# Performance work log

Measured on AMD Instinct MI355X. Metric: run time of the kernel, lower is better.

Reference implementation:

```python
import jax, jax.numpy as jnp
import numpy as np

N_BASIS = 128   # n_atom_basis F
N_INT   = 3     # n_interactions
N_RBF   = 20
CUTOFF  = 5.0
MAX_Z   = 100
EPS     = 1e-8
N_ATOMS = 25000
N_EDGES = 200000


def setup_inputs() -> dict:
    key = jax.random.key(0)
    ks = jax.random.split(key, 16)
    F = N_BASIS
    s = 0.02
    z     = jax.random.randint(ks[0], (N_ATOMS,), 1, MAX_Z)
    pos   = jax.random.uniform(ks[1], (N_ATOMS, 3), dtype=jnp.float32) * 2.0  # small box -> inside cutoff
    idx_i = jax.random.randint(ks[2], (N_EDGES,), 0, N_ATOMS)
    idx_j = jax.random.randint(ks[3], (N_EDGES,), 0, N_ATOMS)
    emb   = jax.random.normal(ks[4], (MAX_Z, F), dtype=jnp.float32) * s
    fW    = jax.random.normal(ks[5], (N_RBF, 3 * F * N_INT), dtype=jnp.float32) * s
    fb    = jnp.zeros((3 * F * N_INT,), jnp.float32)
    iW1   = jax.random.normal(ks[6], (N_INT, F, F), dtype=jnp.float32) * s
    ib1   = jnp.zeros((N_INT, F), jnp.float32)
    iW2   = jax.random.normal(ks[7], (N_INT, F, 3 * F), dtype=jnp.float32) * s
    ib2   = jnp.zeros((N_INT, 3 * F), jnp.float32)
    mWmix = jax.random.normal(ks[8], (N_INT, F, 2 * F), dtype=jnp.float32) * s
    mW1   = jax.random.normal(ks[9], (N_INT, 2 * F, F), dtype=jnp.float32) * s
    mb1   = jnp.zeros((N_INT, F), jnp.float32)
    mW2   = jax.random.normal(ks[10], (N_INT, F, 3 * F), dtype=jnp.float32) * s
    mb2   = jnp.zeros((N_INT, 3 * F), jnp.float32)
    return dict(z=z, pos=pos, idx_i=idx_i, idx_j=idx_j, emb=emb, fW=fW, fb=fb,
                iW1=iW1, ib1=ib1, iW2=iW2, ib2=ib2,
                mWmix=mWmix, mW1=mW1, mb1=mb1, mW2=mW2, mb2=mb2)


def reference(z, pos, idx_i, idx_j, emb, fW, fb, iW1, ib1, iW2, ib2,
              mWmix, mW1, mb1, mW2, mb2):
    F = N_BASIS
    n_atoms = z.shape[0]
    # geometry
    r_ij = pos[idx_j] - pos[idx_i]                                  # [E,3]
    r_ij = jnp.where(jnp.abs(r_ij) < 1e-6, 1e-6, r_ij)
    d_ij = jnp.linalg.norm(r_ij, axis=1, keepdims=True)             # [E,1]
    dir_ij = r_ij / d_ij                                            # [E,3]
    # Gaussian radial basis
    offsets = jnp.linspace(0.0, CUTOFF, N_RBF)
    width = offsets[1] - offsets[0]
    coeff = -0.5 / (width * width)
    phi = jnp.exp(coeff * (d_ij[..., None] - offsets) ** 2)         # [E,1,n_rbf]
    # cosine cutoff
    fcut = 0.5 * (jnp.cos(jnp.pi * d_ij / CUTOFF) + 1.0) * (d_ij < CUTOFF)  # [E,1]
    filters = (phi @ fW + fb) * fcut[..., None]                     # [E,1,3F*I]
    filter_list = jnp.split(filters, N_INT, axis=-1)                # each [E,1,3F]
    # initial atom features
    q = emb[z][:, None, :]                                          # [N,1,F]
    mu = jnp.zeros((n_atoms, 3, F), q.dtype)                        # [N,3,F]
    for t in range(N_INT):
        # --- interaction (gather - filter-multiply - scatter-add) ---
        x = jax.nn.silu(q @ iW1[t] + ib1[t]) @ iW2[t] + ib2[t]      # [N,1,3F]
        xj = x[idx_j]                                               # [E,1,3F]
        muj = mu[idx_j]                                             # [E,3,F]
        x = filter_list[t] * xj                                     # [E,1,3F]
        dq, dmuR, dmumu = jnp.split(x, 3, axis=-1)                  # [E,1,F] each
        dq = jax.ops.segment_sum(dq, idx_i, num_segments=n_atoms)   # [N,1,F]
        dmu = dmuR * dir_ij[..., None] + dmumu * muj                # [E,3,F]
        dmu = jax.ops.segment_sum(dmu, idx_i, num_segments=n_atoms) # [N,3,F]
        q = q + dq
        mu = mu + dmu
        # --- mixing (intra-atomic) ---
        mu_mix = mu @ mWmix[t]                                      # [N,3,2F]
        mu_V, mu_W = jnp.split(mu_mix, 2, axis=-1)                  # [N,3,F]
        mu_Vn = jnp.sqrt(jnp.sum(mu_V ** 2, axis=-2, keepdims=True) + EPS)  # [N,1,F]
        ctx = jnp.concatenate([q, mu_Vn], axis=-1)                  # [N,1,2F]
        x = jax.nn.silu(ctx @ mW1[t] + mb1[t]) @ mW2[t] + mb2[t]    # [N,1,3F]
        dq_intra, dmu_intra, dqmu_intra = jnp.split(x, 3, axis=-1)
        dmu_intra = dmu_intra * mu_W                                # [N,3,F]
        dqmu_intra = dqmu_intra * jnp.sum(mu_V * mu_W, axis=1, keepdims=True)
        q = q + dq_intra + dqmu_intra
        mu = mu + dmu_intra
    return q.squeeze(1), mu
```

## Files before the change

kernel.cpp:

```cpp
#include <hip/hip_runtime.h>
#include <hip/hip_bf16.h>

#define F 128
#define F3 384
#define NRBF 20
#define NITER 3
#define KP 24

typedef __hip_bfloat16 bf16;
typedef __bf16 bfrag __attribute__((ext_vector_type(8)));
typedef float f32x4 __attribute__((ext_vector_type(4)));

__device__ __forceinline__ float b2f(bf16 v) { return __bfloat162float(v); }
__device__ __forceinline__ bf16 f2b(float v) { return __float2bfloat16(v); }
__device__ __forceinline__ bfrag ldb(const bf16* p) { return *(const bfrag*)p; }
__device__ __forceinline__ bfrag ldsb(const __bf16* p) { return *(const bfrag*)p; }
__device__ __forceinline__ bfrag cvtf(const float* p) {
    bfrag r;
#pragma unroll
    for (int j = 0; j < 8; ++j) r[j] = (__bf16)p[j];
    return r;
}

__global__ void detect_kernel(const unsigned short* __restrict__ raw, int n_u16,
                              int* __restrict__ flag) {
    int i = blockIdx.x * blockDim.x + threadIdx.x;
    int bad = 0;
    for (int k = i; k < n_u16; k += blockDim.x * gridDim.x) {
        unsigned e = (raw[k] >> 7) & 0xFFu;
        if (e >= 140u) bad = 1;
    }
    if (bad) atomicOr(flag, 1);
}

struct CvtArgs {
    const void* src[13];
    float* dst[13];
    int end[14];
};
__global__ void cvt_all_kernel(CvtArgs a, const int* __restrict__ flag, int total) {
    int idx = blockIdx.x * blockDim.x + threadIdx.x;
    if (idx >= total) return;
    int s = 0;
    while (idx >= a.end[s + 1]) ++s;
    int local = idx - a.end[s];
    float v = (*flag) ? ((const float*)a.src[s])[local]
                      : b2f(((const bf16*)a.src[s])[local]);
    a.dst[s][local] = v;
}

struct TpArgs {
    const float* src[5];
    bf16* dst[5];
    int K[5];
    int Nn[5];
    int end[6];
};
__global__ void tpose_all_kernel(TpArgs a, int total) {
    int idx = blockIdx.x * blockDim.x + threadIdx.x;
    if (idx >= total) return;
    int s = 0;
    while (idx >= a.end[s + 1]) ++s;
    int local = idx - a.end[s];
    int K = a.K[s], Nn = a.Nn[s], slice = K * Nn;
    int t = local / slice, j = local - t * slice;
    int n = j / K, k = j - n * K;
    a.dst[s][local] = f2b(a.src[s][t * slice + k * Nn + n]);
}

__global__ void fwt_kernel(const float* __restrict__ fW, const float* __restrict__ fb,
                           float* __restrict__ dst, int total) {
    int idx = blockIdx.x * blockDim.x + threadIdx.x;
    if (idx >= total) return;
    int k = idx % KP, rest = idx / KP;
    int n = rest % F3, t = rest / F3;
    float v = (k < NRBF) ? fW[k * (F3 * NITER) + t * F3 + n]
                         : (k == NRBF ? fb[t * F3 + n] : 0.0f);
    dst[idx] = v;
}

__global__ void geom_kernel(const float* __restrict__ pos, const int* __restrict__ ii,
                            const int* __restrict__ jj, const int* __restrict__ rank,
                            bf16* __restrict__ phifc2, float* __restrict__ dir2, int E) {
    int e = blockIdx.x * blockDim.x + threadIdx.x;
    if (e >= E) return;
    int i = ii[e], j = jj[e], l = rank[e];
    float r[3];
#pragma unroll
    for (int d = 0; d < 3; ++d) {
        float v = pos[j * 3 + d] - pos[i * 3 + d];
        if (fabsf(v) < 1e-6f) v = 1e-6f;
        r[d] = v;
    }
    float dd = sqrtf(r[0] * r[0] + r[1] * r[1] + r[2] * r[2]);
    float inv = 1.0f / dd;
#pragma unroll
    for (int d = 0; d < 3; ++d) dir2[(size_t)l * 4 + d] = r[d] * inv;
    dir2[(size_t)l * 4 + 3] = __int_as_float(j);
    const float CUT = 5.0f;
    const float PI = 3.14159265358979323846f;
    float fc = (dd < CUT) ? 0.5f * (cosf(PI * dd / CUT) + 1.0f) : 0.0f;
    const float width = CUT / (NRBF - 1);
    const float coeff = -0.5f / (width * width);
    bf16* pr = phifc2 + (size_t)l * KP;
#pragma unroll
    for (int k = 0; k < NRBF; ++k) {
        float diff = dd - (float)k * width;
        pr[k] = f2b(expf(coeff * diff * diff) * fc);
    }
    pr[NRBF] = f2b(fc);
    pr[NRBF + 1] = f2b(0.0f);
    pr[NRBF + 2] = f2b(0.0f);
    pr[NRBF + 3] = f2b(0.0f);
}

__global__ void embed_kernel(const int* __restrict__ z, const float* __restrict__ emb,
                             float* __restrict__ q, int N) {
    int idx = blockIdx.x * blockDim.x + threadIdx.x;
    if (idx >= N * F) return;
    int n = idx >> 7, f = idx & 127;
    q[idx] = emb[z[n] * F + f];
}

__global__ void count_kernel(const int* __restrict__ ii, int* __restrict__ counts, int E) {
    int e = blockIdx.x * blockDim.x + threadIdx.x;
    if (e < E) atomicAdd(&counts[ii[e]], 1);
}

__global__ void scan_kernel(const int* __restrict__ counts, int* __restrict__ offs, int N) {
    __shared__ int cum[1024];
    int t = threadIdx.x;
    int chunk = (N + 1023) >> 10;
    int b = t * chunk;
    int e = b + chunk; if (e > N) e = N;
    int s = 0;
    for (int a = b; a < e; ++a) s += counts[a];
    cum[t] = s;
    __syncthreads();
    for (int o = 1; o < 1024; o <<= 1) {
        int u = (t >= o) ? cum[t - o] : 0;
        __syncthreads();
        cum[t] += u;
        __syncthreads();
    }
    int run = cum[t] - s;
    for (int a = b; a < e; ++a) { offs[a] = run; run += counts[a]; }
    if (t == 1023) offs[N] = cum[1023];
}

__global__ void fill_kernel(const int* __restrict__ ii, const int* __restrict__ offs,
                            int* __restrict__ cursor, int* __restrict__ rank, int E) {
    int e = blockIdx.x * blockDim.x + threadIdx.x;
    if (e >= E) return;
    int i = ii[e];
    int p = atomicAdd(&cursor[i], 1);
    rank[e] = offs[i] + p;
}

__global__ __launch_bounds__(256) void atom_x_mfma(
    const float* __restrict__ q, const bf16* __restrict__ W1T, const float* __restrict__ b1,
    const bf16* __restrict__ W2T, const float* __restrict__ b2, bf16* __restrict__ x, int N) {
    __shared__ __bf16 H[32][136];
    int tid = threadIdx.x;
    int w = tid >> 6, l = tid & 63;
    int lm = l & 15, q4 = l >> 4;
    int i0 = blockIdx.x * 32;
    f32x4 acc[2][2] = {};
    int r0 = min(i0 + lm, N - 1);
    int r1 = min(i0 + 16 + lm, N - 1);
    for (int kt = 0; kt < 4; ++kt) {
        int ko = kt * 32 + q4 * 8;
        bfrag a0 = cvtf(q + (size_t)r0 * F + ko);
        bfrag a1 = cvtf(q + (size_t)r1 * F + ko);
        bfrag b0 = ldb(W1T + (size_t)(w * 32 + lm) * F + ko);
        bfrag b1f = ldb(W1T + (size_t)(w * 32 + 16 + lm) * F + ko);
        acc[0][0] = __builtin_amdgcn_mfma_f32_16x16x32_bf16(a0, b0, acc[0][0], 0, 0, 0);
        acc[1][0] = __builtin_amdgcn_mfma_f32_16x16x32_bf16(a1, b0, acc[1][0], 0, 0, 0);
        acc[0][1] = __builtin_amdgcn_mfma_f32_16x16x32_bf16(a0, b1f, acc[0][1], 0, 0, 0);
        acc[1][1] = __builtin_amdgcn_mfma_f32_16x16x32_bf16(a1, b1f, acc[1][1], 0, 0, 0);
    }
#pragma unroll
    for (int nt = 0; nt < 2; ++nt) {
        int col = w * 32 + nt * 16 + lm;
        float bb = b1[col];
#pragma unroll
        for (int mt = 0; mt < 2; ++mt)
#pragma unroll
            for (int r = 0; r < 4; ++r) {
                float v = acc[mt][nt][r] + bb;
                H[mt * 16 + q4 * 4 + r][col] = (__bf16)(v / (1.0f + expf(-v)));
            }
    }
    __syncthreads();
#pragma unroll
    for (int j = 0; j < 6; ++j) {
        int n0 = w * 96 + j * 16;
        f32x4 c0 = {}, c1 = {};
        const bf16* bp = W2T + (size_t)(n0 + lm) * F;
        for (int kt = 0; kt < 4; ++kt) {
            int ko = kt * 32 + q4 * 8;
            bfrag a0 = ldsb(&H[lm][ko]);
            bfrag a1 = ldsb(&H[16 + lm][ko]);
            bfrag bf = ldb(bp + ko);
            c0 = __builtin_amdgcn_mfma_f32_16x16x32_bf16(a0, bf, c0, 0, 0, 0);
            c1 = __builtin_amdgcn_mfma_f32_16x16x32_bf16(a1, bf, c1, 0, 0, 0);
        }
        int col = n0 + lm;
        float bb = b2[col];
#pragma unroll
        for (int r = 0; r < 4; ++r) {
            int row0 = i0 + q4 * 4 + r;
            int row1 = row0 + 16;
            if (row0 < N) x[(size_t)row0 * F3 + col] = f2b(c0[r] + bb);
            if (row1 < N) x[(size_t)row1 * F3 + col] = f2b(c1[r] + bb);
        }
    }
}

template<int T0>
__global__ __launch_bounds__(128, 2) void edge_gather_d(
    const bf16* __restrict__ mu_in, const bf16* __restrict__ x,
    const bf16* __restrict__ phifc2, const float* __restrict__ dir2,
    const float* __restrict__ fWTf, const int* __restrict__ offs,
    bf16* __restrict__ dq, bf16* __restrict__ dmu, int N) {
    int i = blockIdx.x;
    int f = threadIdx.x;
    float w0[21], w1[21], w2[21];
    {
        const f32x4* p0 = (const f32x4*)(fWTf + (size_t)f * KP);
        const f32x4* p1 = (const f32x4*)(fWTf + (size_t)(f + 128) * KP);
#pragma unroll
        for (int k = 0; k < 6; ++k) {
            f32x4 t0 = p0[k], t1 = p1[k];
#pragma unroll
            for (int r = 0; r < 4; ++r) {
                int kk = k * 4 + r;
                if (kk < 21) { w0[kk] = t0[r]; w1[kk] = t1[r]; }
            }
        }
        if constexpr (!T0) {
            const f32x4* p2 = (const f32x4*)(fWTf + (size_t)(f + 256) * KP);
#pragma unroll
            for (int k = 0; k < 6; ++k) {
                f32x4 t2 = p2[k];
#pragma unroll
                for (int r = 0; r < 4; ++r) {
                    int kk = k * 4 + r;
                    if (kk < 21) w2[kk] = t2[r];
                }
            }
        }
    }
#pragma unroll
    for (int k = 0; k < 21; ++k) {
        asm volatile("" : "+v"(w0[k]), "+v"(w1[k]));
        if constexpr (!T0) asm volatile("" : "+v"(w2[k]));
    }
    int beg = offs[i], end = offs[i + 1];
    float accq = 0.0f, am0 = 0.0f, am1 = 0.0f, am2 = 0.0f;
    for (int l = beg; l < end; ++l) {
        const bfrag* pb = (const bfrag*)(phifc2 + (size_t)l * KP);
        bfrag p0 = __builtin_nontemporal_load(pb);
        bfrag p1 = __builtin_nontemporal_load(pb + 1);
        bfrag p2 = __builtin_nontemporal_load(pb + 2);
        float ph[21];
#pragma unroll
        for (int k = 0; k < 8; ++k) ph[k] = (float)p0[k];
#pragma unroll
        for (int k = 0; k < 8; ++k) ph[8 + k] = (float)p1[k];
#pragma unroll
        for (int k = 0; k < 5; ++k) ph[16 + k] = (float)p2[k];
        float fl0 = 0.0f, fl1 = 0.0f, fl2 = 0.0f;
#pragma unroll
        for (int k = 0; k < 21; ++k) {
            fl0 += ph[k] * w0[k];
            fl1 += ph[k] * w1[k];
            if constexpr (!T0) fl2 += ph[k] * w2[k];
        }
        f32x4 dv = __builtin_nontemporal_load((const f32x4*)(dir2 + (size_t)l * 4));
        int j = __float_as_int(dv[3]);
        const bf16* xj = x + (size_t)j * F3;
        float dqv = fl0 * b2f(xj[f]);
        float dR = fl1 * b2f(xj[f + 128]);
        accq += dqv;
        if constexpr (!T0) {
            float dM = fl2 * b2f(xj[f + 256]);
            const bf16* muj = mu_in + (size_t)j * F3;
            am0 += dR * dv[0] + dM * b2f(muj[f]);
            am1 += dR * dv[1] + dM * b2f(muj[f + 128]);
            am2 += dR * dv[2] + dM * b2f(muj[f + 256]);
        } else {
            am0 += dR * dv[0];
            am1 += dR * dv[1];
            am2 += dR * dv[2];
        }
    }
    dq[(size_t)i * F + f] = f2b(accq);
    size_t mb = (size_t)i * F3 + f;
    dmu[mb]       = f2b(am0);
    dmu[mb + 128] = f2b(am1);
    dmu[mb + 256] = f2b(am2);
}

template<int T0>
__global__ __launch_bounds__(256) void mixv_mfma(
    const bf16* __restrict__ mu_in, const bf16* __restrict__ dmu,
    const bf16* __restrict__ WmixT,
    bf16* __restrict__ Vn_g, float* __restrict__ S_g, bf16* __restrict__ Wg, int N) {
    __shared__ __bf16 VV[48][131];
    __shared__ __bf16 WW[48][130];
    int tid = threadIdx.x;
    int w = tid >> 6, l = tid & 63;
    int lm = l & 15, q4 = l >> 4;
    int i0 = blockIdx.x * 16;
    int rowsM = N * 3;
    {
        f32x4 acc[3][4] = {};
        int mr[3];
#pragma unroll
        for (int mt = 0; mt < 3; ++mt) mr[mt] = min(i0 * 3 + mt * 16 + lm, rowsM - 1);
        for (int kt = 0; kt < 4; ++kt) {
            int ko = kt * 32 + q4 * 8;
            bfrag a[3], b[4];
#pragma unroll
            for (int mt = 0; mt < 3; ++mt) {
                bfrag d = ldb(dmu + (size_t)mr[mt] * F + ko);
                if constexpr (T0) {
                    a[mt] = d;
                } else {
                    bfrag u = ldb(mu_in + (size_t)mr[mt] * F + ko);
#pragma unroll
                    for (int jj = 0; jj < 8; ++jj)
                        a[mt][jj] = (__bf16)((float)u[jj] + (float)d[jj]);
                }
            }
#pragma unroll
            for (int nt = 0; nt < 4; ++nt)
                b[nt] = ldb(WmixT + (size_t)(w * 64 + nt * 16 + lm) * F + ko);
#pragma unroll
            for (int mt = 0; mt < 3; ++mt)
#pragma unroll
                for (int nt = 0; nt < 4; ++nt)
                    acc[mt][nt] = __builtin_amdgcn_mfma_f32_16x16x32_bf16(a[mt], b[nt], acc[mt][nt], 0, 0, 0);
        }
#pragma unroll
        for (int mt = 0; mt < 3; ++mt)
#pragma unroll
            for (int nt = 0; nt < 4; ++nt) {
                int col = w * 64 + nt * 16 + lm;
#pragma unroll
                for (int r = 0; r < 4; ++r) {
                    int row = mt * 16 + q4 * 4 + r;
                    if (col < 128) VV[row][col] = (__bf16)acc[mt][nt][r];
                    else           WW[row][col - 128] = (__bf16)acc[mt][nt][r];
                }
            }
    }
    __syncthreads();
    for (int idx = tid; idx < 16 * F; idx += 256) {
        int a = idx >> 7, f = idx & 127;
        int i = i0 + a;
        if (i >= N) continue;
        float v0 = (float)VV[a * 3 + 0][f], w0 = (float)WW[a * 3 + 0][f];
        float v1 = (float)VV[a * 3 + 1][f], w1 = (float)WW[a * 3 + 1][f];
        float v2 = (float)VV[a * 3 + 2][f], w2 = (float)WW[a * 3 + 2][f];
        size_t qb = (size_t)i * F + f;
        Vn_g[qb] = f2b(sqrtf(v0 * v0 + v1 * v1 + v2 * v2 + 1e-8f));
        S_g[qb] = v0 * w0 + v1 * w1 + v2 * w2;
        size_t mb = (size_t)i * F3 + f;
        Wg[mb]       = f2b(w0);
        Wg[mb + 128] = f2b(w1);
        Wg[mb + 256] = f2b(w2);
    }
}

template<int T0, int OUT>
__global__ __launch_bounds__(256) void ctx_final(
    float* __restrict__ q, const bf16* __restrict__ dqb,
    const bf16* __restrict__ mu_in, const bf16* __restrict__ dmu,
    const bf16* __restrict__ Vn_g, const float* __restrict__ S_g, const bf16* __restrict__ Wg,
    bf16* __restrict__ mu_out,
    const bf16* __restrict__ W1T, const float* __restrict__ b1,
    const bf16* __restrict__ W2T, const float* __restrict__ b2,
    void* __restrict__ outp, const int* __restrict__ flag, int N) {
    __shared__ __align__(16) char smem[33792];
    __bf16 (*CT)[264] = (__bf16(*)[264])(smem);
    __bf16 (*Y)[392]  = (__bf16(*)[392])(smem);
    __bf16 (*HM)[136] = (__bf16(*)[136])(smem + 25088);
    int tid = threadIdx.x;
    int w = tid >> 6, l = tid & 63;
    int lm = l & 15, q4 = l >> 4;
    int i0 = blockIdx.x * 32;
    for (int idx = tid; idx < 32 * F; idx += 256) {
        int a = idx >> 7, f = idx & 127;
        int i = min(i0 + a, N - 1);
        size_t qb = (size_t)i * F + f;
        float qe = q[qb] + b2f(dqb[qb]);
        CT[a][f] = (__bf16)qe;
        CT[a][F + f] = (__bf16)b2f(Vn_g[qb]);
    }
    __syncthreads();
    {
        f32x4 c0[2] = {}, c1[2] = {};
        for (int kt = 0; kt < 8; ++kt) {
            int ko = kt * 32 + q4 * 8;
            bfrag a0 = ldsb(&CT[lm][ko]);
            bfrag a1 = ldsb(&CT[16 + lm][ko]);
#pragma unroll
            for (int nt = 0; nt < 2; ++nt) {
                bfrag b = ldb(W1T + (size_t)(w * 32 + nt * 16 + lm) * 256 + ko);
                c0[nt] = __builtin_amdgcn_mfma_f32_16x16x32_bf16(a0, b, c0[nt], 0, 0, 0);
                c1[nt] = __builtin_amdgcn_mfma_f32_16x16x32_bf16(a1, b, c1[nt], 0, 0, 0);
            }
        }
#pragma unroll
        for (int nt = 0; nt < 2; ++nt) {
            int col = w * 32 + nt * 16 + lm;
            float bb = b1[col];
#pragma unroll
            for (int r = 0; r < 4; ++r) {
                float v0 = c0[nt][r] + bb;
                float v1 = c1[nt][r] + bb;
                HM[q4 * 4 + r][col] = (__bf16)(v0 / (1.0f + expf(-v0)));
                HM[16 + q4 * 4 + r][col] = (__bf16)(v1 / (1.0f + expf(-v1)));
            }
        }
    }
    __syncthreads();
#pragma unroll
    for (int j = 0; j < 6; ++j) {
        int n0 = w * 96 + j * 16;
        f32x4 c0 = {}, c1 = {};
        const bf16* bp = W2T + (size_t)(n0 + lm) * F;
        for (int kt = 0; kt < 4; ++kt) {
            int ko = kt * 32 + q4 * 8;
            bfrag a0 = ldsb(&HM[lm][ko]);
            bfrag a1 = ldsb(&HM[16 + lm][ko]);
            bfrag b = ldb(bp + ko);
            c0 = __builtin_amdgcn_mfma_f32_16x16x32_bf16(a0, b, c0, 0, 0, 0);
            c1 = __builtin_amdgcn_mfma_f32_16x16x32_bf16(a1, b, c1, 0, 0, 0);
        }
        int col = n0 + lm;
        float bb = b2[col];
#pragma unroll
        for (int r = 0; r < 4; ++r) {
            Y[q4 * 4 + r][col] = (__bf16)(c0[r] + bb);
            Y[16 + q4 * 4 + r][col] = (__bf16)(c1[r] + bb);
        }
    }
    __syncthreads();
    int nq = N * F;
    for (int idx = tid; idx < 32 * F; idx += 256) {
        int a = idx >> 7, f = idx & 127;
        int i = i0 + a;
        if (i >= N) continue;
        size_t qb = (size_t)i * F + f;
        size_t mb = (size_t)i * F3 + f;
        float yq = (float)Y[a][f], ym = (float)Y[a][F + f], ys = (float)Y[a][2 * F + f];
        float s = S_g[qb];
        float W0 = b2f(Wg[mb]);
        float W1v = b2f(Wg[mb + 128]);
        float W2v = b2f(Wg[mb + 256]);
        float qv = q[qb] + b2f(dqb[qb]) + yq + ys * s;
        float m0 = b2f(dmu[mb]);
        float m1 = b2f(dmu[mb + 128]);
        float m2 = b2f(dmu[mb + 256]);
        if constexpr (!T0) {
            m0 += b2f(mu_in[mb]);
            m1 += b2f(mu_in[mb + 128]);
            m2 += b2f(mu_in[mb + 256]);
        }
        m0 += ym * W0;
        m1 += ym * W1v;
        m2 += ym * W2v;
        if constexpr (OUT) {
            if (*flag) {
                float* of = (float*)outp;
                of[qb] = qv;
                of[nq + mb] = m0;
                of[nq + mb + 128] = m1;
                of[nq + mb + 256] = m2;
            } else {
                bf16* ob = (bf16*)outp;
                ob[qb] = f2b(qv);
                ob[nq + mb] = f2b(m0);
                ob[nq + mb + 128] = f2b(m1);
                ob[nq + mb + 256] = f2b(m2);
            }
        } else {
            q[qb] = qv;
            mu_out[mb]       = f2b(m0);
            mu_out[mb + 128] = f2b(m1);
            mu_out[mb + 256] = f2b(m2);
        }
    }
}

extern "C" void kernel_launch(void* const* d_in, const int* in_sizes, int n_in,
                              void* d_out, int out_size, void* d_ws, size_t ws_size,
                              hipStream_t stream) {
    const int* z = (const int*)d_in[0];
    const int* idx_i = (const int*)d_in[2];
    const int* idx_j = (const int*)d_in[3];

    int N = in_sizes[0];
    int E = in_sizes[2];

    char* base = (char*)d_ws;
    size_t off = 0;
    auto alloc = [&](size_t bytes) -> void* {
        void* p = base + off;
        off += (bytes + 255) & ~(size_t)255;
        return p;
    };

    int* flag = (int*)alloc(4);
    float* pos_f = (float*)alloc((size_t)in_sizes[1] * 4);
    float* emb_f = (float*)alloc((size_t)in_sizes[4] * 4);
    float* fW_f = (float*)alloc((size_t)in_sizes[5] * 4);
    float* fb_f = (float*)alloc((size_t)in_sizes[6] * 4);
    float* iW1_f = (float*)alloc((size_t)in_sizes[7] * 4);
    float* ib1_f = (float*)alloc((size_t)in_sizes[8] * 4);
    float* iW2_f = (float*)alloc((size_t)in_sizes[9] * 4);
    float* ib2_f = (float*)alloc((size_t)in_sizes[10] * 4);
    float* mWmix_f = (float*)alloc((size_t)in_sizes[11] * 4);
    float* mW1_f = (float*)alloc((size_t)in_sizes[12] * 4);
    float* mb1_f = (float*)alloc((size_t)in_sizes[13] * 4);
    float* mW2_f = (float*)alloc((size_t)in_sizes[14] * 4);
    float* mb2_f = (float*)alloc((size_t)in_sizes[15] * 4);
    bf16* iW1T = (bf16*)alloc((size_t)NITER * F * F * 2);
    bf16* iW2T = (bf16*)alloc((size_t)NITER * F3 * F * 2);
    bf16* mWmixT = (bf16*)alloc((size_t)NITER * 2 * F * F * 2);
    bf16* mW1T = (bf16*)alloc((size_t)NITER * F * 2 * F * 2);
    bf16* mW2T = (bf16*)alloc((size_t)NITER * F3 * F * 2);
    float* fWTf = (float*)alloc((size_t)NITER * F3 * KP * 4);
    float* q = (float*)alloc((size_t)N * F * 4);
    bf16* dqb = (bf16*)alloc((size_t)N * F * 2);
    bf16* mua = (bf16*)alloc((size_t)N * F3 * 2);
    bf16* mub = (bf16*)alloc((size_t)N * F3 * 2);
    bf16* dmub = (bf16*)alloc((size_t)N * F3 * 2);
    bf16* xbuf = (bf16*)alloc((size_t)N * F3 * 2);
    bf16* Vn_g = (bf16*)alloc((size_t)N * F * 2);
    float* S_g = (float*)alloc((size_t)N * F * 4);
    bf16* Wg = (bf16*)alloc((size_t)N * F3 * 2);
    bf16* phifc2 = (bf16*)alloc((size_t)(E + 16) * KP * 2);
    float* dir2 = (float*)alloc((size_t)(E + 16) * 4 * 4);
    int* rank = (int*)alloc((size_t)E * 4);
    int* counts = (int*)alloc((size_t)N * 4);
    int* offs = (int*)alloc((size_t)(N + 1) * 4);

    hipMemsetAsync(flag, 0, 4, stream);
    detect_kernel<<<64, 256, 0, stream>>>((const unsigned short*)d_in[1], in_sizes[1], flag);

    {
        CvtArgs a;
        const int srcIdx[13] = {1, 4, 5, 6, 7, 8, 9, 10, 11, 12, 13, 14, 15};
        float* dsts[13] = {pos_f, emb_f, fW_f, fb_f, iW1_f, ib1_f, iW2_f, ib2_f,
                           mWmix_f, mW1_f, mb1_f, mW2_f, mb2_f};
        int cum = 0;
        a.end[0] = 0;
        for (int s = 0; s < 13; ++s) {
            a.src[s] = d_in[srcIdx[s]];
            a.dst[s] = dsts[s];
            cum += in_sizes[srcIdx[s]];
            a.end[s + 1] = cum;
        }
        cvt_all_kernel<<<(cum + 255) / 256, 256, 0, stream>>>(a, flag, cum);
    }

    {
        TpArgs a;
        const float* srcs[5] = {iW1_f, iW2_f, mWmix_f, mW1_f, mW2_f};
        bf16* dsts[5] = {iW1T, iW2T, mWmixT, mW1T, mW2T};
        int Ks[5] = {F, F, F, 2 * F, F};
        int Nns[5] = {F, F3, 2 * F, F, F3};
        int cum = 0;
        a.end[0] = 0;
        for (int s = 0; s < 5; ++s) {
            a.src[s] = srcs[s];
            a.dst[s] = dsts[s];
            a.K[s] = Ks[s];
            a.Nn[s] = Nns[s];
            cum += NITER * Ks[s] * Nns[s];
            a.end[s + 1] = cum;
        }
        tpose_all_kernel<<<(cum + 255) / 256, 256, 0, stream>>>(a, cum);
    }
    {
        int total = NITER * F3 * KP;
        fwt_kernel<<<(total + 255) / 256, 256, 0, stream>>>(fW_f, fb_f, fWTf, total);
    }

    hipMemsetAsync(counts, 0, (size_t)N * 4, stream);
    count_kernel<<<(E + 255) / 256, 256, 0, stream>>>(idx_i, counts, E);
    scan_kernel<<<1, 1024, 0, stream>>>(counts, offs, N);
    hipMemsetAsync(counts, 0, (size_t)N * 4, stream);
    fill_kernel<<<(E + 255) / 256, 256, 0, stream>>>(idx_i, offs, counts, rank, E);

    geom_kernel<<<(E + 255) / 256, 256, 0, stream>>>(pos_f, idx_i, idx_j, rank,
                                                     phifc2, dir2, E);
    embed_kernel<<<(N * F + 255) / 256, 256, 0, stream>>>(z, emb_f, q, N);

    int grid16 = (N + 15) / 16;
    int grid32 = (N + 31) / 32;
    bf16* muin = mua;
    bf16* muout = mub;
    atom_x_mfma<<<grid32, 256, 0, stream>>>(q, iW1T, ib1_f, iW2T, ib2_f, xbuf, N);
    edge_gather_d<1><<<N, 128, 0, stream>>>(muin, xbuf, phifc2, dir2,
                                            fWTf, offs, dqb, dmub, N);
    mixv_mfma<1><<<grid16, 256, 0, stream>>>(muin, dmub, mWmixT, Vn_g, S_g, Wg, N);
    ctx_final<1, 0><<<grid32, 256, 0, stream>>>(q, dqb, muin, dmub, Vn_g, S_g, Wg, muout,
                                                mW1T, mb1_f, mW2T, mb2_f,
                                                nullptr, flag, N);
    atom_x_mfma<<<grid32, 256, 0, stream>>>(q, iW1T + (size_t)1 * F * F, ib1_f + 1 * F,
                                            iW2T + (size_t)1 * F3 * F, ib2_f + 1 * F3, xbuf, N);
    { bf16* tm = muin; muin = muout; muout = tm; }
    edge_gather_d<0><<<N, 128, 0, stream>>>(muin, xbuf, phifc2, dir2,
                                            fWTf + (size_t)1 * F3 * KP, offs, dqb, dmub, N);
    mixv_mfma<0><<<grid16, 256, 0, stream>>>(muin, dmub, mWmixT + (size_t)1 * 2 * F * F,
                                             Vn_g, S_g, Wg, N);
    ctx_final<0, 0><<<grid32, 256, 0, stream>>>(q, dqb, muin, dmub, Vn_g, S_g, Wg, muout,
                                                mW1T + (size_t)1 * F * 2 * F, mb1_f + 1 * F,
                                                mW2T + (size_t)1 * F3 * F, mb2_f + 1 * F3,
                                                nullptr, flag, N);
    atom_x_mfma<<<grid32, 256, 0, stream>>>(q, iW1T + (size_t)2 * F * F, ib1_f + 2 * F,
                                            iW2T + (size_t)2 * F3 * F, ib2_f + 2 * F3, xbuf, N);
    { bf16* tm = muin; muin = muout; muout = tm; }
    edge_gather_d<0><<<N, 128, 0, stream>>>(muin, xbuf, phifc2, dir2,
                                            fWTf + (size_t)2 * F3 * KP, offs, dqb, dmub, N);
    mixv_mfma<0><<<grid16, 256, 0, stream>>>(muin, dmub, mWmixT + (size_t)2 * 2 * F * F,
                                             Vn_g, S_g, Wg, N);
    ctx_final<0, 1><<<grid32, 256, 0, stream>>>(q, dqb, muin, dmub, Vn_g, S_g, Wg, muout,
                                                mW1T + (size_t)2 * F * 2 * F, mb1_f + 2 * F,
                                                mW2T + (size_t)2 * F3 * F, mb2_f + 2 * F3,
                                                d_out, flag, N);
}
```

Baseline: 753.4 us.

## Fuse mixing projection and context MLP into one kernel per interaction

Merges the mixv_mfma and ctx_final kernels into a single mix8 kernel that handles 8 atoms per block. V/W projections, the norm and the V·W dot product now stay in shared memory instead of going through global Vn/S/W buffers. This removes one launch per interaction and the global write and read of those intermediates. In exchange each block covers only 8 atoms, so half of every 16-row MFMA tile in the MLP stages is zero padding, and the weight matrices are reloaded by four times as many blocks.

```diff
diff --git a/kernel.cpp b/kernel.cpp
--- a/kernel.cpp
+++ b/kernel.cpp
@@ -302,28 +302,36 @@
     dmu[mb + 256] = f2b(am2);
 }
 
-template<int T0>
-__global__ __launch_bounds__(256) void mixv_mfma(
+template<int T0, int OUT>
+__global__ __launch_bounds__(256) void mix8(
+    float* __restrict__ q, const bf16* __restrict__ dqb,
     const bf16* __restrict__ mu_in, const bf16* __restrict__ dmu,
-    const bf16* __restrict__ WmixT,
-    bf16* __restrict__ Vn_g, float* __restrict__ S_g, bf16* __restrict__ Wg, int N) {
-    __shared__ __bf16 VV[48][131];
-    __shared__ __bf16 WW[48][130];
+    bf16* __restrict__ mu_out,
+    const bf16* __restrict__ WmixT, const bf16* __restrict__ W1T, const float* __restrict__ b1,
+    const bf16* __restrict__ W2T, const float* __restrict__ b2,
+    void* __restrict__ outp, const int* __restrict__ flag, int N) {
+    __shared__ __align__(16) char smem[29568];
+    __bf16 (*WW)[132] = (__bf16(*)[132])(smem);
+    __bf16 (*VV)[132] = (__bf16(*)[132])(smem + 6336);
+    __bf16 (*Y)[392]  = (__bf16(*)[392])(smem + 6336);
+    __bf16 (*CT)[264] = (__bf16(*)[264])(smem + 12672);
+    __bf16 (*HM)[136] = (__bf16(*)[136])(smem + 21120);
+    float  (*SS)[128] = (float(*)[128])(smem + 25472);
     int tid = threadIdx.x;
     int w = tid >> 6, l = tid & 63;
     int lm = l & 15, q4 = l >> 4;
-    int i0 = blockIdx.x * 16;
+    int i0 = blockIdx.x * 8;
     int rowsM = N * 3;
     {
-        f32x4 acc[3][4] = {};
-        int mr[3];
-#pragma unroll
-        for (int mt = 0; mt < 3; ++mt) mr[mt] = min(i0 * 3 + mt * 16 + lm, rowsM - 1);
+        f32x4 acc[2][4] = {};
+        int mr[2];
+        mr[0] = min(i0 * 3 + lm, rowsM - 1);
+        mr[1] = min(i0 * 3 + 16 + lm, rowsM - 1);
         for (int kt = 0; kt < 4; ++kt) {
             int ko = kt * 32 + q4 * 8;
-            bfrag a[3], b[4];
-#pragma unroll
-            for (int mt = 0; mt < 3; ++mt) {
+            bfrag a[2], b[4];
+#pragma unroll
+            for (int mt = 0; mt < 2; ++mt) {
                 bfrag d = ldb(dmu + (size_t)mr[mt] * F + ko);
                 if constexpr (T0) {
                     a[mt] = d;
@@ -338,79 +346,53 @@
             for (int nt = 0; nt < 4; ++nt)
                 b[nt] = ldb(WmixT + (size_t)(w * 64 + nt * 16 + lm) * F + ko);
 #pragma unroll
-            for (int mt = 0; mt < 3; ++mt)
+            for (int mt = 0; mt < 2; ++mt)
 #pragma unroll
                 for (int nt = 0; nt < 4; ++nt)
                     acc[mt][nt] = __builtin_amdgcn_mfma_f32_16x16x32_bf16(a[mt], b[nt], acc[mt][nt], 0, 0, 0);
         }
 #pragma unroll
-        for (int mt = 0; mt < 3; ++mt)
+        for (int mt = 0; mt < 2; ++mt)
 #pragma unroll
             for (int nt = 0; nt < 4; ++nt) {
                 int col = w * 64 + nt * 16 + lm;
 #pragma unroll
                 for (int r = 0; r < 4; ++r) {
                     int row = mt * 16 + q4 * 4 + r;
-                    if (col < 128) VV[row][col] = (__bf16)acc[mt][nt][r];
-                    else           WW[row][col - 128] = (__bf16)acc[mt][nt][r];
+                    if (row < 24) {
+                        if (col < 128) VV[row][col] = (__bf16)acc[mt][nt][r];
+                        else           WW[row][col - 128] = (__bf16)acc[mt][nt][r];
+                    }
                 }
             }
     }
     __syncthreads();
     for (int idx = tid; idx < 16 * F; idx += 256) {
         int a = idx >> 7, f = idx & 127;
-        int i = i0 + a;
-        if (i >= N) continue;
-        float v0 = (float)VV[a * 3 + 0][f], w0 = (float)WW[a * 3 + 0][f];
-        float v1 = (float)VV[a * 3 + 1][f], w1 = (float)WW[a * 3 + 1][f];
-        float v2 = (float)VV[a * 3 + 2][f], w2 = (float)WW[a * 3 + 2][f];
-        size_t qb = (size_t)i * F + f;
-        Vn_g[qb] = f2b(sqrtf(v0 * v0 + v1 * v1 + v2 * v2 + 1e-8f));
-        S_g[qb] = v0 * w0 + v1 * w1 + v2 * w2;
-        size_t mb = (size_t)i * F3 + f;
-        Wg[mb]       = f2b(w0);
-        Wg[mb + 128] = f2b(w1);
-        Wg[mb + 256] = f2b(w2);
-    }
-}
-
-template<int T0, int OUT>
-__global__ __launch_bounds__(256) void ctx_final(
-    float* __restrict__ q, const bf16* __restrict__ dqb,
-    const bf16* __restrict__ mu_in, const bf16* __restrict__ dmu,
-    const bf16* __restrict__ Vn_g, const float* __restrict__ S_g, const bf16* __restrict__ Wg,
-    bf16* __restrict__ mu_out,
-    const bf16* __restrict__ W1T, const float* __restrict__ b1,
-    const bf16* __restrict__ W2T, const float* __restrict__ b2,
-    void* __restrict__ outp, const int* __restrict__ flag, int N) {
-    __shared__ __align__(16) char smem[33792];
-    __bf16 (*CT)[264] = (__bf16(*)[264])(smem);
-    __bf16 (*Y)[392]  = (__bf16(*)[392])(smem);
-    __bf16 (*HM)[136] = (__bf16(*)[136])(smem + 25088);
-    int tid = threadIdx.x;
-    int w = tid >> 6, l = tid & 63;
-    int lm = l & 15, q4 = l >> 4;
-    int i0 = blockIdx.x * 32;
-    for (int idx = tid; idx < 32 * F; idx += 256) {
-        int a = idx >> 7, f = idx & 127;
-        int i = min(i0 + a, N - 1);
-        size_t qb = (size_t)i * F + f;
-        float qe = q[qb] + b2f(dqb[qb]);
-        CT[a][f] = (__bf16)qe;
-        CT[a][F + f] = (__bf16)b2f(Vn_g[qb]);
+        if (a < 8) {
+            int i = min(i0 + a, N - 1);
+            float v0 = (float)VV[a * 3 + 0][f], ww0 = (float)WW[a * 3 + 0][f];
+            float v1 = (float)VV[a * 3 + 1][f], ww1 = (float)WW[a * 3 + 1][f];
+            float v2 = (float)VV[a * 3 + 2][f], ww2 = (float)WW[a * 3 + 2][f];
+            SS[a][f] = v0 * ww0 + v1 * ww1 + v2 * ww2;
+            size_t qb = (size_t)i * F + f;
+            CT[a][f] = (__bf16)(q[qb] + b2f(dqb[qb]));
+            CT[a][F + f] = (__bf16)sqrtf(v0 * v0 + v1 * v1 + v2 * v2 + 1e-8f);
+        } else {
+            CT[a][f] = (__bf16)0.0f;
+            CT[a][F + f] = (__bf16)0.0f;
+        }
     }
     __syncthreads();
     {
-        f32x4 c0[2] = {}, c1[2] = {};
+        f32x4 c[2] = {};
         for (int kt = 0; kt < 8; ++kt) {
             int ko = kt * 32 + q4 * 8;
-            bfrag a0 = ldsb(&CT[lm][ko]);
-            bfrag a1 = ldsb(&CT[16 + lm][ko]);
+            bfrag a = ldsb(&CT[lm][ko]);
 #pragma unroll
             for (int nt = 0; nt < 2; ++nt) {
                 bfrag b = ldb(W1T + (size_t)(w * 32 + nt * 16 + lm) * 256 + ko);
-                c0[nt] = __builtin_amdgcn_mfma_f32_16x16x32_bf16(a0, b, c0[nt], 0, 0, 0);
-                c1[nt] = __builtin_amdgcn_mfma_f32_16x16x32_bf16(a1, b, c1[nt], 0, 0, 0);
+                c[nt] = __builtin_amdgcn_mfma_f32_16x16x32_bf16(a, b, c[nt], 0, 0, 0);
             }
         }
 #pragma unroll
@@ -419,10 +401,8 @@
             float bb = b1[col];
 #pragma unroll
             for (int r = 0; r < 4; ++r) {
-                float v0 = c0[nt][r] + bb;
-                float v1 = c1[nt][r] + bb;
-                HM[q4 * 4 + r][col] = (__bf16)(v0 / (1.0f + expf(-v0)));
-                HM[16 + q4 * 4 + r][col] = (__bf16)(v1 / (1.0f + expf(-v1)));
+                float v = c[nt][r] + bb;
+                HM[q4 * 4 + r][col] = (__bf16)(v / (1.0f + expf(-v)));
             }
         }
     }
@@ -430,37 +410,35 @@
 #pragma unroll
     for (int j = 0; j < 6; ++j) {
         int n0 = w * 96 + j * 16;
-        f32x4 c0 = {}, c1 = {};
+        f32x4 c = {};
         const bf16* bp = W2T + (size_t)(n0 + lm) * F;
         for (int kt = 0; kt < 4; ++kt) {
             int ko = kt * 32 + q4 * 8;
-            bfrag a0 = ldsb(&HM[lm][ko]);
-            bfrag a1 = ldsb(&HM[16 + lm][ko]);
+            bfrag a = ldsb(&HM[lm][ko]);
             bfrag b = ldb(bp + ko);
-            c0 = __builtin_amdgcn_mfma_f32_16x16x32_bf16(a0, b, c0, 0, 0, 0);
-            c1 = __builtin_amdgcn_mfma_f32_16x16x32_bf16(a1, b, c1, 0, 0, 0);
+            c = __builtin_amdgcn_mfma_f32_16x16x32_bf16(a, b, c, 0, 0, 0);
         }
         int col = n0 + lm;
         float bb = b2[col];
 #pragma unroll
         for (int r = 0; r < 4; ++r) {
-            Y[q4 * 4 + r][col] = (__bf16)(c0[r] + bb);
-            Y[16 + q4 * 4 + r][col] = (__bf16)(c1[r] + bb);
+            int row = q4 * 4 + r;
+            if (row < 8) Y[row][col] = (__bf16)(c[r] + bb);
         }
     }
     __syncthreads();
     int nq = N * F;
-    for (int idx = tid; idx < 32 * F; idx += 256) {
+    for (int idx = tid; idx < 8 * F; idx += 256) {
         int a = idx >> 7, f = idx & 127;
         int i = i0 + a;
         if (i >= N) continue;
         size_t qb = (size_t)i * F + f;
         size_t mb = (size_t)i * F3 + f;
         float yq = (float)Y[a][f], ym = (float)Y[a][F + f], ys = (float)Y[a][2 * F + f];
-        float s = S_g[qb];
-        float W0 = b2f(Wg[mb]);
-        float W1v = b2f(Wg[mb + 128]);
-        float W2v = b2f(Wg[mb + 256]);
+        float s = SS[a][f];
+        float W0 = (float)WW[a * 3 + 0][f];
+        float W1v = (float)WW[a * 3 + 1][f];
+        float W2v = (float)WW[a * 3 + 2][f];
         float qv = q[qb] + b2f(dqb[qb]) + yq + ys * s;
         float m0 = b2f(dmu[mb]);
         float m1 = b2f(dmu[mb + 128]);
@@ -540,9 +518,6 @@
     bf16* mub = (bf16*)alloc((size_t)N * F3 * 2);
     bf16* dmub = (bf16*)alloc((size_t)N * F3 * 2);
     bf16* xbuf = (bf16*)alloc((size_t)N * F3 * 2);
-    bf16* Vn_g = (bf16*)alloc((size_t)N * F * 2);
-    float* S_g = (float*)alloc((size_t)N * F * 4);
-    bf16* Wg = (bf16*)alloc((size_t)N * F3 * 2);
     bf16* phifc2 = (bf16*)alloc((size_t)(E + 16) * KP * 2);
     float* dir2 = (float*)alloc((size_t)(E + 16) * 4 * 4);
     int* rank = (int*)alloc((size_t)E * 4);
@@ -601,37 +576,34 @@
                                                      phifc2, dir2, E);
     embed_kernel<<<(N * F + 255) / 256, 256, 0, stream>>>(z, emb_f, q, N);
 
-    int grid16 = (N + 15) / 16;
+    int grid8 = (N + 7) / 8;
     int grid32 = (N + 31) / 32;
     bf16* muin = mua;
     bf16* muout = mub;
     atom_x_mfma<<<grid32, 256, 0, stream>>>(q, iW1T, ib1_f, iW2T, ib2_f, xbuf, N);
     edge_gather_d<1><<<N, 128, 0, stream>>>(muin, xbuf, phifc2, dir2,
                                             fWTf, offs, dqb, dmub, N);
-    mixv_mfma<1><<<grid16, 256, 0, stream>>>(muin, dmub, mWmixT, Vn_g, S_g, Wg, N);
-    ctx_final<1, 0><<<grid32, 256, 0, stream>>>(q, dqb, muin, dmub, Vn_g, S_g, Wg, muout,
-                                                mW1T, mb1_f, mW2T, mb2_f,
-                                                nullptr, flag, N);
+    mix8<1, 0><<<grid8, 256, 0, stream>>>(q, dqb, muin, dmub, muout,
+                                          mWmixT, mW1T, mb1_f, mW2T, mb2_f,
+                                          nullptr, flag, N);
     atom_x_mfma<<<grid32, 256, 0, stream>>>(q, iW1T + (size_t)1 * F * F, ib1_f + 1 * F,
                                             iW2T + (size_t)1 * F3 * F, ib2_f + 1 * F3, xbuf, N);
     { bf16* tm = muin; muin = muout; muout = tm; }
     edge_gather_d<0><<<N, 128, 0, stream>>>(muin, xbuf, phifc2, dir2,
                                             fWTf + (size_t)1 * F3 * KP, offs, dqb, dmub, N);
-    mixv_mfma<0><<<grid16, 256, 0, stream>>>(muin, dmub, mWmixT + (size_t)1 * 2 * F * F,
-                                             Vn_g, S_g, Wg, N);
-    ctx_final<0, 0><<<grid32, 256, 0, stream>>>(q, dqb, muin, dmub, Vn_g, S_g, Wg, muout,
-                                                mW1T + (size_t)1 * F * 2 * F, mb1_f + 1 * F,
-                                                mW2T + (size_t)1 * F3 * F, mb2_f + 1 * F3,
-                                                nullptr, flag, N);
+    mix8<0, 0><<<grid8, 256, 0, stream>>>(q, dqb, muin, dmub, muout,
+                                          mWmixT + (size_t)1 * 2 * F * F,
+                                          mW1T + (size_t)1 * F * 2 * F, mb1_f + 1 * F,
+                                          mW2T + (size_t)1 * F3 * F, mb2_f + 1 * F3,
+                                          nullptr, flag, N);
     atom_x_mfma<<<grid32, 256, 0, stream>>>(q, iW1T + (size_t)2 * F * F, ib1_f + 2 * F,
                                             iW2T + (size_t)2 * F3 * F, ib2_f + 2 * F3, xbuf, N);
     { bf16* tm = muin; muin = muout; muout = tm; }
     edge_gather_d<0><<<N, 128, 0, stream>>>(muin, xbuf, phifc2, dir2,
                                             fWTf + (size_t)2 * F3 * KP, offs, dqb, dmub, N);
-    mixv_mfma<0><<<grid16, 256, 0, stream>>>(muin, dmub, mWmixT + (size_t)2 * 2 * F * F,
-                                             Vn_g, S_g, Wg, N);
-    ctx_final<0, 1><<<grid32, 256, 0, stream>>>(q, dqb, muin, dmub, Vn_g, S_g, Wg, muout,
-                                                mW1T + (size_t)2 * F * 2 * F, mb1_f + 2 * F,
-                                                mW2T + (size_t)2 * F3 * F, mb2_f + 2 * F3,
-                                                d_out, flag, N);
-}
+    mix8<0, 1><<<grid8, 256, 0, stream>>>(q, dqb, muin, dmub, muout,
+                                          mWmixT + (size_t)2 * 2 * F * F,
+                                          mW1T + (size_t)2 * F * 2 * F, mb1_f + 2 * F,
+                                          mW2T + (size_t)2 * F3 * F, mb2_f + 2 * F3,
+                                          d_out, flag, N);
+}
```

Result: slower. 868.4 us (+15.3%).
